# Optimization experiments

Measured on AMD Instinct MI355X. Metric: run time of the kernel, lower is better.

The kernel has to match this reference:

```python
import jax, jax.numpy as jnp
import numpy as np

CONF_THRES = 0.25
IOU_THRES = 0.45
MAX_DET = 1000
MAX_WH = 4096.0  # class offset used by YOLOv5 for class-aware NMS
K = 1024         # fixed candidate count (static-shape stand-in for conf filtering)


def xywh2xyxy(b):
    cx, cy, w, h = b[..., 0], b[..., 1], b[..., 2], b[..., 3]
    return jnp.stack([cx - w / 2, cy - h / 2, cx + w / 2, cy + h / 2], axis=-1)


def pairwise_iou(boxes):
    # boxes: [K,4] xyxy -> [K,K] IoU
    x1, y1, x2, y2 = boxes[:, 0], boxes[:, 1], boxes[:, 2], boxes[:, 3]
    area = (x2 - x1) * (y2 - y1)
    ix1 = jnp.maximum(x1[:, None], x1[None, :])
    iy1 = jnp.maximum(y1[:, None], y1[None, :])
    ix2 = jnp.minimum(x2[:, None], x2[None, :])
    iy2 = jnp.minimum(y2[:, None], y2[None, :])
    inter = jnp.clip(ix2 - ix1, 0.0) * jnp.clip(iy2 - iy1, 0.0)
    return inter / (area[:, None] + area[None, :] - inter + 1e-9)


def nms_image(pred):
    # pred: [N, 5+nc] = xywh, obj, class scores
    boxes = xywh2xyxy(pred[:, :4])                 # [N,4]
    scores = pred[:, 5:] * pred[:, 4:5]            # conf = obj * cls
    conf = jnp.max(scores, axis=-1)                # [N]
    cls = jnp.argmax(scores, axis=-1)              # [N] int
    masked = jnp.where(conf > CONF_THRES, conf, -1.0)
    top_conf, idx = jax.lax.top_k(masked, K)       # sorted desc
    cand_boxes = boxes[idx]                        # [K,4]
    cand_cls = cls[idx]                            # [K]
    cand_valid = top_conf > 0.0                    # below-threshold slots are -1
    # class-aware NMS: offset boxes per class so different classes never overlap
    off_boxes = cand_boxes + (cand_cls.astype(pred.dtype) * MAX_WH)[:, None]
    iou = pairwise_iou(off_boxes)                  # [K,K]

    def step(suppressed, i):
        keep_i = jnp.logical_and(jnp.logical_not(suppressed[i]), cand_valid[i])
        suppressed = jnp.where(keep_i, jnp.logical_or(suppressed, iou[i] > IOU_THRES), suppressed)
        return suppressed, keep_i

    _, keep = jax.lax.scan(step, jnp.zeros((K,), dtype=bool), jnp.arange(K))
    sel_score = jnp.where(keep, top_conf, -1.0)
    fin_score, fin_idx = jax.lax.top_k(sel_score, MAX_DET)
    ok = fin_score > 0.0
    det = jnp.concatenate(
        [cand_boxes[fin_idx],
         top_conf[fin_idx][:, None],
         cand_cls[fin_idx].astype(pred.dtype)[:, None]],
        axis=-1,
    )  # [MAX_DET, 6] = x1,y1,x2,y2,conf,cls
    return jnp.where(ok[:, None], det, 0.0)


def setup_inputs() -> dict:
    key = jax.random.key(0)
    k1, k2, k3, k4 = jax.random.split(key, 4)
    B, N, NC = 16, 25200, 80
    cxcy = jax.random.uniform(k1, (B, N, 2), dtype=jnp.float32) * 640.0
    wh = jax.random.uniform(k2, (B, N, 2), dtype=jnp.float32) * 96.0 + 4.0
    obj = jax.random.uniform(k3, (B, N, 1), dtype=jnp.float32)
    cls = jax.random.uniform(k4, (B, N, NC), dtype=jnp.float32)
    pred = jnp.concatenate([cxcy, wh, obj, cls], axis=-1)
    return {"pred": pred}


def reference(pred):
    # [B, MAX_DET, 6] zero-padded detections per image
    return jax.vmap(nms_image)(pred)
```

## Files before the change

### kernel.cpp

```cpp
#include <hip/hip_runtime.h>
#include <stdint.h>

typedef unsigned int u32;
typedef unsigned long long u64;

#define BB 16
#define NN 25200
#define ROWLEN 85
#define KCAND 1024
#define MAXDET 1000
#define CONF_T 0.25f
#define IOU_T 0.45f
#define MAX_WH 4096.0f
#define KBASE 0xBE800000u

__device__ __forceinline__ u32 f2key(float f) {
  u32 u = __float_as_uint(f);
  return (u & 0x80000000u) ? ~u : (u | 0x80000000u);
}
__device__ __forceinline__ float key2f(u32 k) {
  u32 u = (k & 0x80000000u) ? (k & 0x7FFFFFFFu) : ~k;
  return __uint_as_float(u);
}

__global__ __launch_bounds__(64) void k_score(const float* __restrict__ pred,
                                              float* __restrict__ masked,
                                              int* __restrict__ clsArr) {
  __shared__ float sh[64 * ROWLEN];
  const int t = threadIdx.x;
  const size_t blk = (size_t)blockIdx.x;
  const float4* src = (const float4*)(pred + blk * (64 * ROWLEN));
  float4* dst = (float4*)sh;
  #pragma unroll
  for (int i = 0; i < 21; ++i) dst[t + 64 * i] = src[t + 64 * i];
  if (t < 16) dst[t + 64 * 21] = src[t + 64 * 21];
  __syncthreads();
  const float* row = sh + t * ROWLEN;
  float obj = row[4];
  float v0 = -INFINITY, v1 = -INFINITY, v2 = -INFINITY, v3 = -INFINITY;
  int j0 = 0, j1 = 20, j2 = 40, j3 = 60;
  #pragma unroll
  for (int c = 0; c < 20; ++c) {
    float s0 = obj * row[5 + c];
    float s1 = obj * row[25 + c];
    float s2 = obj * row[45 + c];
    float s3 = obj * row[65 + c];
    if (s0 > v0) { v0 = s0; j0 = c; }
    if (s1 > v1) { v1 = s1; j1 = 20 + c; }
    if (s2 > v2) { v2 = s2; j2 = 40 + c; }
    if (s3 > v3) { v3 = s3; j3 = 60 + c; }
  }
  float v = v0; int j = j0;
  if (v1 > v) { v = v1; j = j1; }
  if (v2 > v) { v = v2; j = j2; }
  if (v3 > v) { v = v3; j = j3; }
  size_t r = blk * 64 + t;
  masked[r] = (v > CONF_T) ? v : -1.0f;
  clsArr[r] = j;
}

__device__ __forceinline__ void bt_apply(u64& e, u64 p, int m, int j, int k) {
  bool lower = ((m & j) == 0);
  bool dir = ((m & k) == 0);
  bool takeMax = (lower == dir);
  u64 mx = e > p ? e : p;
  u64 mn = e > p ? p : e;
  e = takeMax ? mx : mn;
}

__global__ __launch_bounds__(1024, 4) void k_select(const float* __restrict__ pred,
                                                    const float* __restrict__ masked,
                                                    const int* __restrict__ clsArr,
                                                    float* __restrict__ candScore,
                                                    float* __restrict__ candBox,
                                                    int* __restrict__ candCls) {
  __shared__ u32 hist[16][257];
  __shared__ u64 buf[2048];
  __shared__ u32 sh_sel, sh_rem, sh_cnt;
  const int b = blockIdx.x;
  const int tid = threadIdx.x;
  const int lane = tid & 63;
  const int wv = tid >> 6;
  const float* m = masked + (size_t)b * NN;
  u32* histflat = (u32*)hist;

  u32 rr[25];
  #pragma unroll
  for (int it = 0; it < 25; ++it) {
    int n0 = tid + it * 1024;
    float val = (n0 < NN) ? m[n0] : -1.0f;
    u32 r = f2key(val) - KBASE;
    rr[it] = (val > 0.0f) ? r : 0u;
  }

  u32 prefix = 0, himask = 0, remaining = KCAND;
  #pragma unroll
  for (int pass = 0; pass < 3; ++pass) {
    int shift = 16 - 8 * pass;
    for (int i = tid; i < 16 * 257; i += 1024) histflat[i] = 0;
    __syncthreads();
    #pragma unroll
    for (int it = 0; it < 25; ++it) {
      u32 r = rr[it];
      if (r != 0u && (r & himask) == prefix)
        atomicAdd(&hist[wv][(r >> shift) & 255], 1u);
    }
    __syncthreads();
    if (wv == 0) {
      u32 c0 = 0, c1 = 0, c2 = 0, c3 = 0;
      #pragma unroll
      for (int w = 0; w < 16; ++w) {
        c0 += hist[w][4 * lane + 0];
        c1 += hist[w][4 * lane + 1];
        c2 += hist[w][4 * lane + 2];
        c3 += hist[w][4 * lane + 3];
      }
      u32 tl = c0 + c1 + c2 + c3;
      u32 incl = tl;
      #pragma unroll
      for (int off = 1; off <= 32; off <<= 1) {
        u32 o = __shfl_down(incl, off, 64);
        if (lane + off < 64) incl += o;
      }
      u32 S0 = incl;
      u32 S1 = S0 - c0;
      u32 S2 = S1 - c1;
      u32 S3 = S2 - c2;
      u32 S4 = S3 - c3;
      u32 rem = remaining;
      if (S0 >= rem && S1 < rem) { sh_sel = 4 * lane + 0; sh_rem = rem - S1; }
      if (S1 >= rem && S2 < rem) { sh_sel = 4 * lane + 1; sh_rem = rem - S2; }
      if (S2 >= rem && S3 < rem) { sh_sel = 4 * lane + 2; sh_rem = rem - S3; }
      if (S3 >= rem && S4 < rem) { sh_sel = 4 * lane + 3; sh_rem = rem - S4; }
    }
    __syncthreads();
    prefix |= (sh_sel << shift);
    remaining = sh_rem;
    himask |= (0xFFu << shift);
    __syncthreads();
  }
  const u32 T = prefix;
  if (tid == 0) sh_cnt = 0;
  __syncthreads();
  #pragma unroll
  for (int it = 0; it < 25; ++it) {
    int n0 = tid + it * 1024;
    u32 r = rr[it];
    bool match = (r >= T);
    u64 bal = __ballot(match);
    if (bal) {
      int leader = __ffsll((unsigned long long)bal) - 1;
      u32 base = 0;
      u32 cnt = (u32)__popcll(bal);
      if (lane == leader) base = atomicAdd(&sh_cnt, cnt);
      base = __shfl(base, leader, 64);
      if (match) {
        u32 pos = base + (u32)__popcll(bal & ((1ull << lane) - 1ull));
        if (pos < 2048) buf[pos] = ((u64)r << 32) | (u32)(~(u32)n0);
      }
    }
  }
  __syncthreads();
  u32 c = sh_cnt; if (c > 2048) c = 2048;
  for (int t = tid; t < 2048; t += 1024) if (t >= (int)c) buf[t] = 0;
  __syncthreads();

  u64 e0 = buf[tid];
  u64 e1 = buf[tid + 1024];
  #pragma unroll
  for (int k = 2; k <= 64; k <<= 1) {
    #pragma unroll
    for (int j = k >> 1; j > 0; j >>= 1) {
      u64 p0 = __shfl_xor(e0, j, 64);
      u64 p1 = __shfl_xor(e1, j, 64);
      bt_apply(e0, p0, tid, j, k);
      bt_apply(e1, p1, tid + 1024, j, k);
    }
  }
  for (int k = 128; k <= 2048; k <<= 1) {
    int jstart = k >> 1;
    if (k == 2048) {
      u64 mx = e0 > e1 ? e0 : e1;
      u64 mn = e0 > e1 ? e1 : e0;
      e0 = mx; e1 = mn;
      jstart = 512;
    }
    for (int j = jstart; j >= 64; j >>= 1) {
      buf[tid] = e0; buf[tid + 1024] = e1;
      __syncthreads();
      u64 p0 = buf[tid ^ j];
      u64 p1 = buf[(tid ^ j) + 1024];
      bt_apply(e0, p0, tid, j, k);
      bt_apply(e1, p1, tid + 1024, j, k);
      __syncthreads();
    }
    #pragma unroll
    for (int j = 32; j > 0; j >>= 1) {
      u64 p0 = __shfl_xor(e0, j, 64);
      u64 p1 = __shfl_xor(e1, j, 64);
      bt_apply(e0, p0, tid, j, k);
      bt_apply(e1, p1, tid + 1024, j, k);
    }
  }
  {
    u64 e = e0;
    u32 r = (u32)(e >> 32);
    u32 idx = ~(u32)e;
    if (idx >= NN) idx = 0;
    float sc = key2f(r + KBASE);
    size_t g = (size_t)b * KCAND + tid;
    candScore[g] = sc;
    const float* p = pred + ((size_t)b * NN + idx) * ROWLEN;
    float cx = p[0], cy = p[1], w = p[2], h = p[3];
    float4 bx;
    bx.x = cx - 0.5f * w;
    bx.y = cy - 0.5f * h;
    bx.z = cx + 0.5f * w;
    bx.w = cy + 0.5f * h;
    ((float4*)candBox)[g] = bx;
    candCls[g] = clsArr[(size_t)b * NN + idx];
  }
}

__global__ __launch_bounds__(256) void k_iou(const float* __restrict__ candBox,
                                             const int* __restrict__ candCls,
                                             u64* __restrict__ matT) {
  #pragma clang fp contract(off)
  __shared__ float sx1[KCAND], sy1[KCAND], sx2[KCAND], sy2[KCAND], sar[KCAND];
  const int b = blockIdx.y;
  const int r0 = blockIdx.x * 64;
  const int tid = threadIdx.x;
  for (int i = tid; i < KCAND; i += 256) {
    float4 bx = ((const float4*)candBox)[(size_t)b * KCAND + i];
    float off = (float)candCls[(size_t)b * KCAND + i] * MAX_WH;
    float x1 = bx.x + off, y1 = bx.y + off, x2 = bx.z + off, y2 = bx.w + off;
    sx1[i] = x1; sy1[i] = y1; sx2[i] = x2; sy2[i] = y2;
    sar[i] = (x2 - x1) * (y2 - y1);
  }
  __syncthreads();
  const int row = r0 + (tid & 63);
  const int wbase = tid >> 6;
  float rx1 = sx1[row], ry1 = sy1[row], rx2 = sx2[row], ry2 = sy2[row], rar = sar[row];
  for (int q = 0; q < 4; ++q) {
    int w = wbase + q * 4;
    int jb = w << 6;
    u64 mk = 0;
    for (int kk = 0; kk < 64; ++kk) {
      int jj = jb + kk;
      float ix1 = fmaxf(rx1, sx1[jj]);
      float iy1 = fmaxf(ry1, sy1[jj]);
      float ix2 = fminf(rx2, sx2[jj]);
      float iy2 = fminf(ry2, sy2[jj]);
      float dx = fmaxf(ix2 - ix1, 0.0f);
      float dy = fmaxf(iy2 - iy1, 0.0f);
      float inter = dx * dy;
      float den = rar + sar[jj];
      den = den - inter;
      den = den + 1e-9f;
      float iou = inter / den;
      if (iou > IOU_T) mk |= (1ull << kk);
    }
    matT[(((size_t)b * 16 + w) << 10) + row] = mk;
  }
}

#define TRIDX(c, cp) (((c) * ((c)-1)) / 2 + (cp))
__global__ __launch_bounds__(256, 1) void k_scan_out(const u64* __restrict__ matT,
                                                     const float* __restrict__ candScore,
                                                     const float* __restrict__ candBox,
                                                     const int* __restrict__ candCls,
                                                     float* __restrict__ out) {
  __shared__ u64 sKeep[16];
  const int b = blockIdx.x;
  const int tid = threadIdx.x;
  const u64* Mb = matT + ((size_t)b << 14);

  if (tid < 64) {
    const int lane = tid;
    u64 vw[16], dg[16], tri[120], kcw[16];
    #pragma unroll
    for (int w = 0; w < 16; ++w) {
      float sc = candScore[(size_t)b * KCAND + w * 64 + lane];
      vw[w] = __ballot(sc > 0.0f);
    }
    #pragma unroll
    for (int c = 0; c < 16; ++c)
      dg[c] = Mb[((size_t)c << 10) + c * 64 + lane];
    #pragma unroll
    for (int c = 1; c < 16; ++c) {
      #pragma unroll
      for (int cp = 0; cp < c; ++cp)
        tri[TRIDX(c, cp)] = Mb[((size_t)c << 10) + cp * 64 + lane];
    }

    #pragma unroll
    for (int c = 0; c < 16; ++c) {
      u64 acc = 0;
      #pragma unroll
      for (int cp = 0; cp < 15; ++cp) {
        if (cp < c) {
          if ((kcw[cp] >> lane) & 1ull) acc |= tri[TRIDX(c, cp)];
        }
      }
      #pragma unroll
      for (int st = 1; st < 64; st <<= 1) acc |= __shfl_xor(acc, st, 64);
      u64 d = dg[c];
      u64 s = acc;
      u64 kc = 0;
      u64 vc = vw[c];
      #pragma unroll
      for (int g = 0; g < 8; ++g) {
        u64 dgp[8];
        #pragma unroll
        for (int j = 0; j < 8; ++j) dgp[j] = __shfl(d, g * 8 + j, 64);
        #pragma unroll
        for (int j = 0; j < 8; ++j) {
          int i = g * 8 + j;
          bool ok = !((s >> i) & 1ull) && ((vc >> i) & 1ull);
          if (ok) { s |= dgp[j]; kc |= (1ull << i); }
        }
      }
      kcw[c] = kc;
    }
    if (lane < 16) sKeep[lane] = kcw[lane];
  }
  __syncthreads();

  int total = 0;
  #pragma unroll
  for (int w = 0; w < 16; ++w) total += __popcll(sKeep[w]);
  int kept_eff = total < MAXDET ? total : MAXDET;
  float* outb = out + (size_t)b * MAXDET * 6;
  #pragma unroll
  for (int rr2 = 0; rr2 < 4; ++rr2) {
    const int t = tid + rr2 * 256;
    u64 word = sKeep[t >> 6];
    int bit = (int)((word >> (t & 63)) & 1ull);
    int rank = 0;
    for (int w = 0; w < (t >> 6); ++w) rank += __popcll(sKeep[w]);
    rank += __popcll(word & ((1ull << (t & 63)) - 1ull));
    if (bit && rank < MAXDET) {
      size_t g = (size_t)b * KCAND + t;
      float4 bx = ((const float4*)candBox)[g];
      float sc = candScore[g];
      float cf = (float)candCls[g];
      float* o = outb + (size_t)rank * 6;
      o[0] = bx.x; o[1] = bx.y; o[2] = bx.z; o[3] = bx.w; o[4] = sc; o[5] = cf;
    }
    if (t < MAXDET && t >= kept_eff) {
      float* o = outb + (size_t)t * 6;
      o[0] = 0.f; o[1] = 0.f; o[2] = 0.f; o[3] = 0.f; o[4] = 0.f; o[5] = 0.f;
    }
  }
}

extern "C" void kernel_launch(void* const* d_in, const int* in_sizes, int n_in,
                              void* d_out, int out_size, void* d_ws, size_t ws_size,
                              hipStream_t stream) {
  const float* pred = (const float*)d_in[0];
  float* out = (float*)d_out;
  char* ws = (char*)d_ws;
  size_t o = 0;
  float* masked    = (float*)(ws + o); o += (size_t)BB * NN * 4;
  int*   clsArr    = (int*)  (ws + o); o += (size_t)BB * NN * 4;
  float* candScore = (float*)(ws + o); o += (size_t)BB * KCAND * 4;
  float* candBox   = (float*)(ws + o); o += (size_t)BB * KCAND * 16;
  int*   candCls   = (int*)  (ws + o); o += (size_t)BB * KCAND * 4;
  o = (o + 255) & ~(size_t)255;
  u64*   matT      = (u64*)  (ws + o); o += (size_t)BB * KCAND * 16 * 8;

  const int rows = BB * NN;
  k_score<<<rows / 64, 64, 0, stream>>>(pred, masked, clsArr);
  k_select<<<BB, 1024, 0, stream>>>(pred, masked, clsArr, candScore, candBox, candCls);
  k_iou<<<dim3(16, BB), 256, 0, stream>>>(candBox, candCls, matT);
  k_scan_out<<<BB, 256, 0, stream>>>(matT, candScore, candBox, candCls, out);
}
```

Before: 310.3 us.

## Fuse first radix-select histogram into scoring; compute only upper-triangle IoU tiles

The scoring kernel now emits radix keys directly and builds per-block 256-bin histograms of the top key byte. The select kernel reduces these instead of running its own first histogram pass, and it loads keys as uint4. The IoU kernel now runs on 64x64 tiles and skips tiles below the diagonal, packing rows with wave ballots, so it does about half the pairwise work. The cost is extra global traffic for the per-block histograms and many tiny blocks in the IoU launch, and it relies on the scan kernel only reading upper-triangle words.

Result: slower. 332.6 us (+7.2%).

```diff
diff --git a/kernel.cpp b/kernel.cpp
--- a/kernel.cpp
+++ b/kernel.cpp
@@ -13,6 +13,7 @@
 #define IOU_T 0.45f
 #define MAX_WH 4096.0f
 #define KBASE 0xBE800000u
+#define NBLK 394
 
 __device__ __forceinline__ u32 f2key(float f) {
   u32 u = __float_as_uint(f);
@@ -24,39 +25,55 @@
 }
 
 __global__ __launch_bounds__(64) void k_score(const float* __restrict__ pred,
-                                              float* __restrict__ masked,
-                                              int* __restrict__ clsArr) {
+                                              u32* __restrict__ keys,
+                                              int* __restrict__ clsArr,
+                                              u32* __restrict__ gh) {
   __shared__ float sh[64 * ROWLEN];
+  __shared__ u32 h[256];
   const int t = threadIdx.x;
-  const size_t blk = (size_t)blockIdx.x;
-  const float4* src = (const float4*)(pred + blk * (64 * ROWLEN));
+  const int bi = blockIdx.x;
+  const int img = blockIdx.y;
+  const int r0 = bi * 64;
+  const int nrows = (r0 + 64 <= NN) ? 64 : (NN - r0);
+  const int nf4 = nrows * ROWLEN / 4;
+  const float4* src = (const float4*)(pred + ((size_t)img * NN + r0) * ROWLEN);
   float4* dst = (float4*)sh;
-  #pragma unroll
-  for (int i = 0; i < 21; ++i) dst[t + 64 * i] = src[t + 64 * i];
-  if (t < 16) dst[t + 64 * 21] = src[t + 64 * 21];
-  __syncthreads();
-  const float* row = sh + t * ROWLEN;
-  float obj = row[4];
-  float v0 = -INFINITY, v1 = -INFINITY, v2 = -INFINITY, v3 = -INFINITY;
-  int j0 = 0, j1 = 20, j2 = 40, j3 = 60;
-  #pragma unroll
-  for (int c = 0; c < 20; ++c) {
-    float s0 = obj * row[5 + c];
-    float s1 = obj * row[25 + c];
-    float s2 = obj * row[45 + c];
-    float s3 = obj * row[65 + c];
-    if (s0 > v0) { v0 = s0; j0 = c; }
-    if (s1 > v1) { v1 = s1; j1 = 20 + c; }
-    if (s2 > v2) { v2 = s2; j2 = 40 + c; }
-    if (s3 > v3) { v3 = s3; j3 = 60 + c; }
-  }
-  float v = v0; int j = j0;
-  if (v1 > v) { v = v1; j = j1; }
-  if (v2 > v) { v = v2; j = j2; }
-  if (v3 > v) { v = v3; j = j3; }
-  size_t r = blk * 64 + t;
-  masked[r] = (v > CONF_T) ? v : -1.0f;
-  clsArr[r] = j;
+  h[t] = 0u; h[t + 64] = 0u; h[t + 128] = 0u; h[t + 192] = 0u;
+  for (int i = t; i < nf4; i += 64) dst[i] = src[i];
+  __syncthreads();
+  if (t < nrows) {
+    const float* row = sh + t * ROWLEN;
+    float obj = row[4];
+    float v0 = -INFINITY, v1 = -INFINITY, v2 = -INFINITY, v3 = -INFINITY;
+    int j0 = 0, j1 = 20, j2 = 40, j3 = 60;
+    #pragma unroll
+    for (int c = 0; c < 20; ++c) {
+      float s0 = obj * row[5 + c];
+      float s1 = obj * row[25 + c];
+      float s2 = obj * row[45 + c];
+      float s3 = obj * row[65 + c];
+      if (s0 > v0) { v0 = s0; j0 = c; }
+      if (s1 > v1) { v1 = s1; j1 = 20 + c; }
+      if (s2 > v2) { v2 = s2; j2 = 40 + c; }
+      if (s3 > v3) { v3 = s3; j3 = 60 + c; }
+    }
+    float v = v0; int j = j0;
+    if (v1 > v) { v = v1; j = j1; }
+    if (v2 > v) { v = v2; j = j2; }
+    if (v3 > v) { v = v3; j = j3; }
+    u32 key = 0u;
+    if (v > CONF_T) {
+      key = f2key(v) - KBASE;
+      atomicAdd(&h[key >> 16], 1u);
+    }
+    size_t r = (size_t)img * NN + r0 + t;
+    keys[r] = key;
+    clsArr[r] = j;
+  }
+  __syncthreads();
+  u32* outp = gh + ((size_t)img * NBLK + bi) * 256;
+  outp[t] = h[t]; outp[t + 64] = h[t + 64];
+  outp[t + 128] = h[t + 128]; outp[t + 192] = h[t + 192];
 }
 
 __device__ __forceinline__ void bt_apply(u64& e, u64 p, int m, int j, int k) {
@@ -69,52 +86,88 @@
 }
 
 __global__ __launch_bounds__(1024, 4) void k_select(const float* __restrict__ pred,
-                                                    const float* __restrict__ masked,
+                                                    const u32* __restrict__ keys,
                                                     const int* __restrict__ clsArr,
+                                                    const u32* __restrict__ gh,
                                                     float* __restrict__ candScore,
                                                     float* __restrict__ candBox,
                                                     int* __restrict__ candCls) {
-  __shared__ u32 hist[16][257];
+  __shared__ u32 hist4[4][256];
+  __shared__ u32 hist1[257];
   __shared__ u64 buf[2048];
   __shared__ u32 sh_sel, sh_rem, sh_cnt;
   const int b = blockIdx.x;
   const int tid = threadIdx.x;
   const int lane = tid & 63;
   const int wv = tid >> 6;
-  const float* m = masked + (size_t)b * NN;
-  u32* histflat = (u32*)hist;
-
-  u32 rr[25];
-  #pragma unroll
-  for (int it = 0; it < 25; ++it) {
-    int n0 = tid + it * 1024;
-    float val = (n0 < NN) ? m[n0] : -1.0f;
-    u32 r = f2key(val) - KBASE;
-    rr[it] = (val > 0.0f) ? r : 0u;
-  }
+
+  u32 rr[28];
+  const uint4* k4 = (const uint4*)(keys + (size_t)b * NN);
+  #pragma unroll
+  for (int it = 0; it < 7; ++it) {
+    int i4 = tid + (it << 10);
+    uint4 q = make_uint4(0u, 0u, 0u, 0u);
+    if (i4 < (NN >> 2)) q = k4[i4];
+    rr[4 * it + 0] = q.x; rr[4 * it + 1] = q.y;
+    rr[4 * it + 2] = q.z; rr[4 * it + 3] = q.w;
+  }
+
+  {
+    const int bin = tid & 255;
+    const int part = tid >> 8;
+    u32 csum = 0;
+    const u32* g = gh + ((size_t)b * NBLK) * 256 + bin;
+    for (int s = part; s < NBLK; s += 4) csum += g[(size_t)s << 8];
+    hist4[part][bin] = csum;
+  }
+  if (tid == 0) sh_cnt = 0;
+  __syncthreads();
 
   u32 prefix = 0, himask = 0, remaining = KCAND;
-  #pragma unroll
-  for (int pass = 0; pass < 3; ++pass) {
-    int shift = 16 - 8 * pass;
-    for (int i = tid; i < 16 * 257; i += 1024) histflat[i] = 0;
+  if (wv == 0) {
+    const int j4 = lane << 2;
+    u32 c0 = hist4[0][j4 + 0] + hist4[1][j4 + 0] + hist4[2][j4 + 0] + hist4[3][j4 + 0];
+    u32 c1 = hist4[0][j4 + 1] + hist4[1][j4 + 1] + hist4[2][j4 + 1] + hist4[3][j4 + 1];
+    u32 c2 = hist4[0][j4 + 2] + hist4[1][j4 + 2] + hist4[2][j4 + 2] + hist4[3][j4 + 2];
+    u32 c3 = hist4[0][j4 + 3] + hist4[1][j4 + 3] + hist4[2][j4 + 3] + hist4[3][j4 + 3];
+    u32 tl = c0 + c1 + c2 + c3;
+    u32 incl = tl;
+    #pragma unroll
+    for (int off = 1; off <= 32; off <<= 1) {
+      u32 o = __shfl_down(incl, off, 64);
+      if (lane + off < 64) incl += o;
+    }
+    u32 S0 = incl;
+    u32 S1 = S0 - c0;
+    u32 S2 = S1 - c1;
+    u32 S3 = S2 - c2;
+    u32 S4 = S3 - c3;
+    u32 rem = remaining;
+    if (S0 >= rem && S1 < rem) { sh_sel = 4 * lane + 0; sh_rem = rem - S1; }
+    if (S1 >= rem && S2 < rem) { sh_sel = 4 * lane + 1; sh_rem = rem - S2; }
+    if (S2 >= rem && S3 < rem) { sh_sel = 4 * lane + 2; sh_rem = rem - S3; }
+    if (S3 >= rem && S4 < rem) { sh_sel = 4 * lane + 3; sh_rem = rem - S4; }
+  }
+  __syncthreads();
+  prefix = (sh_sel << 16);
+  remaining = sh_rem;
+  himask = 0xFF0000u;
+
+  #pragma unroll
+  for (int pass = 1; pass < 3; ++pass) {
+    const int shift = 16 - 8 * pass;
+    if (tid < 256) hist1[tid] = 0u;
     __syncthreads();
     #pragma unroll
-    for (int it = 0; it < 25; ++it) {
+    for (int it = 0; it < 28; ++it) {
       u32 r = rr[it];
       if (r != 0u && (r & himask) == prefix)
-        atomicAdd(&hist[wv][(r >> shift) & 255], 1u);
+        atomicAdd(&hist1[(r >> shift) & 255], 1u);
     }
     __syncthreads();
     if (wv == 0) {
-      u32 c0 = 0, c1 = 0, c2 = 0, c3 = 0;
-      #pragma unroll
-      for (int w = 0; w < 16; ++w) {
-        c0 += hist[w][4 * lane + 0];
-        c1 += hist[w][4 * lane + 1];
-        c2 += hist[w][4 * lane + 2];
-        c3 += hist[w][4 * lane + 3];
-      }
+      const int j4 = lane << 2;
+      u32 c0 = hist1[j4 + 0], c1 = hist1[j4 + 1], c2 = hist1[j4 + 2], c3 = hist1[j4 + 3];
       u32 tl = c0 + c1 + c2 + c3;
       u32 incl = tl;
       #pragma unroll
@@ -140,11 +193,9 @@
     __syncthreads();
   }
   const u32 T = prefix;
-  if (tid == 0) sh_cnt = 0;
-  __syncthreads();
-  #pragma unroll
-  for (int it = 0; it < 25; ++it) {
-    int n0 = tid + it * 1024;
+
+  #pragma unroll
+  for (int it = 0; it < 28; ++it) {
     u32 r = rr[it];
     bool match = (r >= T);
     u64 bal = __ballot(match);
@@ -155,6 +206,7 @@
       if (lane == leader) base = atomicAdd(&sh_cnt, cnt);
       base = __shfl(base, leader, 64);
       if (match) {
+        int n0 = ((tid + ((it >> 2) << 10)) << 2) + (it & 3);
         u32 pos = base + (u32)__popcll(bal & ((1ull << lane) - 1ull));
         if (pos < 2048) buf[pos] = ((u64)r << 32) | (u32)(~(u32)n0);
       }
@@ -222,46 +274,51 @@
   }
 }
 
-__global__ __launch_bounds__(256) void k_iou(const float* __restrict__ candBox,
-                                             const int* __restrict__ candCls,
-                                             u64* __restrict__ matT) {
+__global__ __launch_bounds__(64) void k_iou(const float* __restrict__ candBox,
+                                            const int* __restrict__ candCls,
+                                            u64* __restrict__ matT) {
   #pragma clang fp contract(off)
-  __shared__ float sx1[KCAND], sy1[KCAND], sx2[KCAND], sy2[KCAND], sar[KCAND];
-  const int b = blockIdx.y;
-  const int r0 = blockIdx.x * 64;
-  const int tid = threadIdx.x;
-  for (int i = tid; i < KCAND; i += 256) {
-    float4 bx = ((const float4*)candBox)[(size_t)b * KCAND + i];
-    float off = (float)candCls[(size_t)b * KCAND + i] * MAX_WH;
+  __shared__ float4 sb[64];
+  __shared__ float sa[64];
+  const int rc = blockIdx.x;
+  const int cc = blockIdx.y;
+  const int b  = blockIdx.z;
+  if (rc > cc) return;
+  const int lane = threadIdx.x;
+  {
+    int rrow = rc * 64 + lane;
+    float4 bx = ((const float4*)candBox)[(size_t)b * KCAND + rrow];
+    float off = (float)candCls[(size_t)b * KCAND + rrow] * MAX_WH;
     float x1 = bx.x + off, y1 = bx.y + off, x2 = bx.z + off, y2 = bx.w + off;
-    sx1[i] = x1; sy1[i] = y1; sx2[i] = x2; sy2[i] = y2;
-    sar[i] = (x2 - x1) * (y2 - y1);
-  }
-  __syncthreads();
-  const int row = r0 + (tid & 63);
-  const int wbase = tid >> 6;
-  float rx1 = sx1[row], ry1 = sy1[row], rx2 = sx2[row], ry2 = sy2[row], rar = sar[row];
-  for (int q = 0; q < 4; ++q) {
-    int w = wbase + q * 4;
-    int jb = w << 6;
-    u64 mk = 0;
-    for (int kk = 0; kk < 64; ++kk) {
-      int jj = jb + kk;
-      float ix1 = fmaxf(rx1, sx1[jj]);
-      float iy1 = fmaxf(ry1, sy1[jj]);
-      float ix2 = fminf(rx2, sx2[jj]);
-      float iy2 = fminf(ry2, sy2[jj]);
-      float dx = fmaxf(ix2 - ix1, 0.0f);
-      float dy = fmaxf(iy2 - iy1, 0.0f);
-      float inter = dx * dy;
-      float den = rar + sar[jj];
-      den = den - inter;
-      den = den + 1e-9f;
-      float iou = inter / den;
-      if (iou > IOU_T) mk |= (1ull << kk);
-    }
-    matT[(((size_t)b * 16 + w) << 10) + row] = mk;
-  }
+    float4 sbv; sbv.x = x1; sbv.y = y1; sbv.z = x2; sbv.w = y2;
+    sb[lane] = sbv;
+    sa[lane] = (x2 - x1) * (y2 - y1);
+  }
+  int col = cc * 64 + lane;
+  float4 cb = ((const float4*)candBox)[(size_t)b * KCAND + col];
+  float coff = (float)candCls[(size_t)b * KCAND + col] * MAX_WH;
+  float cx1 = cb.x + coff, cy1 = cb.y + coff, cx2 = cb.z + coff, cy2 = cb.w + coff;
+  float car = (cx2 - cx1) * (cy2 - cy1);
+  __syncthreads();
+  u64 myw = 0;
+  for (int r = 0; r < 64; ++r) {
+    float4 rb = sb[r];
+    float ra = sa[r];
+    float ix1 = fmaxf(rb.x, cx1);
+    float iy1 = fmaxf(rb.y, cy1);
+    float ix2 = fminf(rb.z, cx2);
+    float iy2 = fminf(rb.w, cy2);
+    float dx = fmaxf(ix2 - ix1, 0.0f);
+    float dy = fmaxf(iy2 - iy1, 0.0f);
+    float inter = dx * dy;
+    float den = ra + car;
+    den = den - inter;
+    den = den + 1e-9f;
+    float iou = inter / den;
+    u64 bal = __ballot(iou > IOU_T);
+    if (lane == r) myw = bal;
+  }
+  matT[(((size_t)b * 16 + cc) << 10) + rc * 64 + lane] = myw;
 }
 
 #define TRIDX(c, cp) (((c) * ((c)-1)) / 2 + (cp))
@@ -361,17 +418,17 @@
   float* out = (float*)d_out;
   char* ws = (char*)d_ws;
   size_t o = 0;
-  float* masked    = (float*)(ws + o); o += (size_t)BB * NN * 4;
+  u32*   keysW     = (u32*)  (ws + o); o += (size_t)BB * NN * 4;
   int*   clsArr    = (int*)  (ws + o); o += (size_t)BB * NN * 4;
+  u32*   gh        = (u32*)  (ws + o); o += (size_t)BB * NBLK * 256 * 4;
   float* candScore = (float*)(ws + o); o += (size_t)BB * KCAND * 4;
   float* candBox   = (float*)(ws + o); o += (size_t)BB * KCAND * 16;
   int*   candCls   = (int*)  (ws + o); o += (size_t)BB * KCAND * 4;
   o = (o + 255) & ~(size_t)255;
   u64*   matT      = (u64*)  (ws + o); o += (size_t)BB * KCAND * 16 * 8;
 
-  const int rows = BB * NN;
-  k_score<<<rows / 64, 64, 0, stream>>>(pred, masked, clsArr);
-  k_select<<<BB, 1024, 0, stream>>>(pred, masked, clsArr, candScore, candBox, candCls);
-  k_iou<<<dim3(16, BB), 256, 0, stream>>>(candBox, candCls, matT);
+  k_score<<<dim3(NBLK, BB), 64, 0, stream>>>(pred, keysW, clsArr, gh);
+  k_select<<<BB, 1024, 0, stream>>>(pred, keysW, clsArr, gh, candScore, candBox, candCls);
+  k_iou<<<dim3(16, 16, BB), 64, 0, stream>>>(candBox, candCls, matT);
   k_scan_out<<<BB, 256, 0, stream>>>(matT, candScore, candBox, candCls, out);
 }
```
